# Performance work log

Hardware: AMD Instinct MI355X
Metric: run time of the kernel (lower is better)

The kernel has to match this reference:

```python
import jax, jax.numpy as jnp
import numpy as np

CROP_H = 14
CROP_W = 14
EXTRAPOLATION_VALUE = 0.0


def setup_inputs() -> dict:
    key = jax.random.key(0)
    k1, k2, k3 = jax.random.split(key, 3)
    image = jax.random.normal(k1, (8, 256, 100, 152), dtype=jnp.float32)
    # normalized box coords in [0,1]; (y1,x1,y2,x2), y2<y1 allowed (extrapolation handles it)
    boxes = jax.random.uniform(k2, (1000, 4), dtype=jnp.float32)
    box_ind = jax.random.randint(k3, (1000,), 0, 8, dtype=jnp.int32)
    return {"image": image, "boxes": boxes, "box_ind": box_ind}


def _crop_and_resize(image, boxes, box_ind):
    # image: [B, C, H, W]; boxes: [N, 4] (y1, x1, y2, x2) normalized; box_ind: [N]
    B, C, H, W = image.shape
    dt = image.dtype
    y1, x1, y2, x2 = boxes[:, 0], boxes[:, 1], boxes[:, 2], boxes[:, 3]

    # TF crop_and_resize sampling grid (crop size > 1 path)
    h_scale = (y2 - y1) * (H - 1) / (CROP_H - 1)          # [N]
    w_scale = (x2 - x1) * (W - 1) / (CROP_W - 1)          # [N]
    in_y = y1[:, None] * (H - 1) + jnp.arange(CROP_H, dtype=dt)[None, :] * h_scale[:, None]  # [N, ch]
    in_x = x1[:, None] * (W - 1) + jnp.arange(CROP_W, dtype=dt)[None, :] * w_scale[:, None]  # [N, cw]

    valid_y = (in_y >= 0) & (in_y <= H - 1)               # [N, ch]
    valid_x = (in_x >= 0) & (in_x <= W - 1)               # [N, cw]

    top = jnp.floor(in_y)
    left = jnp.floor(in_x)
    y_lerp = in_y - top                                    # [N, ch]
    x_lerp = in_x - left                                   # [N, cw]

    ti = jnp.clip(top, 0, H - 1).astype(jnp.int32)         # top index    [N, ch]
    bi = jnp.clip(top + 1, 0, H - 1).astype(jnp.int32)     # bottom index [N, ch]
    li = jnp.clip(left, 0, W - 1).astype(jnp.int32)        # left index   [N, cw]
    ri = jnp.clip(left + 1, 0, W - 1).astype(jnp.int32)    # right index  [N, cw]

    b = box_ind[:, None, None]                             # [N, 1, 1]
    yt = ti[:, :, None]
    yb = bi[:, :, None]
    xl = li[:, None, :]
    xr = ri[:, None, :]

    # mixed advanced indexing -> gathered dims first: [N, ch, cw, C]
    tl = image[b, :, yt, xl]
    tr = image[b, :, yt, xr]
    bl = image[b, :, yb, xl]
    br = image[b, :, yb, xr]

    xw = x_lerp[:, None, :, None]                          # [N, 1, cw, 1]
    yw = y_lerp[:, :, None, None]                          # [N, ch, 1, 1]
    top_v = tl + (tr - tl) * xw
    bot_v = bl + (br - bl) * xw
    val = top_v + (bot_v - top_v) * yw                     # [N, ch, cw, C]

    valid = (valid_y[:, :, None] & valid_x[:, None, :])[..., None]
    out = jnp.where(valid, val, jnp.asarray(EXTRAPOLATION_VALUE, dt))
    return jnp.transpose(out, (0, 3, 1, 2))                # [N, C, ch, cw]


def reference(image, boxes, box_ind):
    return _crop_and_resize(image, boxes, box_ind)
```

## Files before the change

### kernel.cpp

```cpp
#include <hip/hip_runtime.h>

#define CROP_H 14
#define CROP_W 14
#define IMG_B 8
#define IMG_C 256
#define IMG_H 100
#define IMG_W 152
#define NBOX 1000
#define PLANE (IMG_H * IMG_W)
#define POS (CROP_H * CROP_W)
#define OUT_PER_BOX (IMG_C * POS)
#define CG 32
#define NCG (IMG_C / CG)

typedef float f2u __attribute__((ext_vector_type(2), aligned(4)));

__global__ __launch_bounds__(1024) void sort_boxes_kernel(
    const int* __restrict__ box_ind,
    int* __restrict__ perm)
{
    __shared__ unsigned s_mask[IMG_B][32];
    __shared__ int s_tot[IMG_B];
    const int tid = threadIdx.x;

    if (tid < IMG_B * 32) ((unsigned*)s_mask)[tid] = 0u;
    __syncthreads();

    int key = 0;
    if (tid < NBOX) {
        key = box_ind[tid];
        atomicOr(&s_mask[key][tid >> 5], 1u << (tid & 31));
    }
    __syncthreads();

    if (tid < IMG_B) {
        int t = 0;
        #pragma unroll
        for (int w = 0; w < 32; ++w) t += __popc(s_mask[tid][w]);
        s_tot[tid] = t;
    }
    __syncthreads();

    if (tid < NBOX) {
        int base = 0;
        #pragma unroll
        for (int k = 0; k < IMG_B; ++k) base += (k < key) ? s_tot[k] : 0;
        const int w = tid >> 5, b = tid & 31;
        int r = __popc(s_mask[key][w] & ((b == 0) ? 0u : ((1u << b) - 1u)));
        for (int ww = 0; ww < w; ++ww) r += __popc(s_mask[key][ww]);
        perm[base + r] = tid;
    }
}

__global__ __launch_bounds__(256) void CropAndResize_16630113370849_kernel(
    const float* __restrict__ image,
    const float* __restrict__ boxes,
    const int* __restrict__ box_ind,
    const int* __restrict__ perm,
    int use_perm,
    float* __restrict__ out)
{
    const int bid  = blockIdx.x;
    const int cg   = bid & 7;
    const int slot = bid >> 3;
    const int tid  = threadIdx.x;
    if (tid >= POS) return;

    const int n = use_perm ? perm[slot] : slot;
    const int b = box_ind[n];

    const int y = tid / CROP_W;
    const int x = tid - y * CROP_W;

    const float y1 = boxes[n * 4 + 0];
    const float x1 = boxes[n * 4 + 1];
    const float y2 = boxes[n * 4 + 2];
    const float x2 = boxes[n * 4 + 3];

    const float hs   = __fdiv_rn(__fmul_rn(__fsub_rn(y2, y1), (float)(IMG_H - 1)),
                                 (float)(CROP_H - 1));
    const float in_y = __fadd_rn(__fmul_rn(y1, (float)(IMG_H - 1)),
                                 __fmul_rn((float)y, hs));
    const int vy = (in_y >= 0.0f) && (in_y <= (float)(IMG_H - 1));
    const float top = floorf(in_y);
    const float yw  = __fsub_rn(in_y, top);
    const int ti = (int)fminf(fmaxf(top, 0.0f), (float)(IMG_H - 1));

    const float ws   = __fdiv_rn(__fmul_rn(__fsub_rn(x2, x1), (float)(IMG_W - 1)),
                                 (float)(CROP_W - 1));
    const float in_x = __fadd_rn(__fmul_rn(x1, (float)(IMG_W - 1)),
                                 __fmul_rn((float)x, ws));
    const int vx = (in_x >= 0.0f) && (in_x <= (float)(IMG_W - 1));
    const float left = floorf(in_x);
    const float xw   = __fsub_rn(in_x, left);
    const int li = (int)fminf(fmaxf(left, 0.0f), (float)(IMG_W - 1));

    const int r0   = min(ti, IMG_H - 2);
    const int c0   = min(li, IMG_W - 2);
    const bool sely = (ti == IMG_H - 1);
    const bool selx = (li == IMG_W - 1);
    const bool vald = (vy & vx) != 0;

    const float* __restrict__ pl =
        image + (size_t)b * (size_t)(IMG_C * PLANE)
              + (size_t)(cg * CG) * PLANE + (r0 * IMG_W + c0);
    float* __restrict__ po =
        out + (size_t)n * (size_t)OUT_PER_BOX + (size_t)(cg * CG) * POS + tid;

    #pragma unroll 8
    for (int cl = 0; cl < CG; ++cl) {
        const f2u ra = *(const f2u*)(pl);
        const f2u rb = *(const f2u*)(pl + IMG_W);

        const float tA = sely ? rb.x : ra.x;
        const float tB = sely ? rb.y : ra.y;
        const float tl = selx ? tB : tA;
        const float bl = selx ? rb.y : rb.x;

        const float top_v = __fadd_rn(tl, __fmul_rn(__fsub_rn(tB, tl), xw));
        const float bot_v = __fadd_rn(bl, __fmul_rn(__fsub_rn(rb.y, bl), xw));
        const float v = __fadd_rn(top_v, __fmul_rn(__fsub_rn(bot_v, top_v), yw));

        __builtin_nontemporal_store(vald ? v : 0.0f, po);
        pl += PLANE;
        po += POS;
    }
}

extern "C" void kernel_launch(void* const* d_in, const int* in_sizes, int n_in,
                              void* d_out, int out_size, void* d_ws, size_t ws_size,
                              hipStream_t stream) {
    const float* image  = (const float*)d_in[0];
    const float* boxes  = (const float*)d_in[1];
    const int*   boxind = (const int*)d_in[2];
    float* out = (float*)d_out;

    const int use_perm = (ws_size >= (size_t)(NBOX * sizeof(int))) ? 1 : 0;
    int* perm = (int*)d_ws;

    if (use_perm) {
        sort_boxes_kernel<<<1, 1024, 0, stream>>>(boxind, perm);
    }

    dim3 grid(NBOX * NCG);
    dim3 block(256);
    CropAndResize_16630113370849_kernel<<<grid, block, 0, stream>>>(
        image, boxes, boxind, perm, use_perm, out);
}
```

Measured before the change: 104.0 us.

## Transpose image to channel-last layout and gather via coalesced HWC crop kernel

Adds a transpose kernel that rewrites the image into a per-64-channel-group HWC layout in workspace. A new crop kernel then gathers the four corner rows as contiguous 64-channel vectors per sample position, with one lane per channel, and stages results in shared memory so the NCHW output stores are coalesced. The aim is to replace the scattered per-channel 8-byte gathers of the old CHW path. The cost is an extra full-image read and write on every call, plus a dependence on a large workspace; if the workspace is too small, the old path runs with plain stores.

```diff
diff --git a/kernel.cpp b/kernel.cpp
--- a/kernel.cpp
+++ b/kernel.cpp
@@ -12,6 +12,9 @@
 #define OUT_PER_BOX (IMG_C * POS)
 #define CG 32
 #define NCG (IMG_C / CG)
+#define G64 4
+#define IMGT_BYTES ((size_t)IMG_B * G64 * PLANE * 64 * 4)
+#define WS_NEED (IMGT_BYTES + NBOX * sizeof(int))
 
 typedef float f2u __attribute__((ext_vector_type(2), aligned(4)));
 
@@ -52,7 +55,140 @@
     }
 }
 
-__global__ __launch_bounds__(256) void CropAndResize_16630113370849_kernel(
+__global__ __launch_bounds__(256) void transpose_kernel(
+    const float* __restrict__ img, float* __restrict__ imgT)
+{
+    __shared__ float tile[64][65];
+    const int pos0 = blockIdx.x * 64;
+    const int g = blockIdx.y, b = blockIdx.z;
+    const int lane = threadIdx.x & 63, warp = threadIdx.x >> 6;
+
+    const int pos_r = pos0 + lane;
+    #pragma unroll
+    for (int i = 0; i < 16; ++i) {
+        const int cl = warp * 16 + i;
+        float v = 0.0f;
+        if (pos_r < PLANE)
+            v = img[((size_t)(b * IMG_C + g * 64 + cl)) * PLANE + pos_r];
+        tile[lane][cl] = v;
+    }
+    __syncthreads();
+    #pragma unroll
+    for (int i = 0; i < 16; ++i) {
+        const int pl = warp * 16 + i;
+        const int pos = pos0 + pl;
+        if (pos < PLANE)
+            imgT[(((size_t)(b * G64 + g)) * PLANE + pos) * 64 + lane] = tile[pl][lane];
+    }
+}
+
+__global__ __launch_bounds__(256) void crop_hwc_kernel(
+    const float* __restrict__ imgT,
+    const float* __restrict__ boxes,
+    const int* __restrict__ box_ind,
+    const int* __restrict__ perm,
+    float* __restrict__ out)
+{
+    __shared__ int   s_pack[POS];
+    __shared__ float s_xw[POS], s_yw[POS];
+    __shared__ float stile[28][65];
+
+    const int bid  = blockIdx.x;
+    const int k    = bid & 7;
+    const int g    = k & 3;
+    const int slot = (k >> 2) * 500 + (bid >> 3);
+    const int tid  = threadIdx.x;
+    const int lane = tid & 63, warp = tid >> 6;
+
+    const int n = perm[slot];
+    const int b = box_ind[n];
+
+    if (tid < POS) {
+        const int y = tid / CROP_W;
+        const int x = tid - y * CROP_W;
+
+        const float y1 = boxes[n * 4 + 0];
+        const float x1 = boxes[n * 4 + 1];
+        const float y2 = boxes[n * 4 + 2];
+        const float x2 = boxes[n * 4 + 3];
+
+        const float hs   = __fdiv_rn(__fmul_rn(__fsub_rn(y2, y1), (float)(IMG_H - 1)),
+                                     (float)(CROP_H - 1));
+        const float in_y = __fadd_rn(__fmul_rn(y1, (float)(IMG_H - 1)),
+                                     __fmul_rn((float)y, hs));
+        const int vy = (in_y >= 0.0f) && (in_y <= (float)(IMG_H - 1));
+        const float top = floorf(in_y);
+        const float ylp = __fsub_rn(in_y, top);
+        const int ti = (int)fminf(fmaxf(top, 0.0f), (float)(IMG_H - 1));
+
+        const float ws   = __fdiv_rn(__fmul_rn(__fsub_rn(x2, x1), (float)(IMG_W - 1)),
+                                     (float)(CROP_W - 1));
+        const float in_x = __fadd_rn(__fmul_rn(x1, (float)(IMG_W - 1)),
+                                     __fmul_rn((float)x, ws));
+        const int vx = (in_x >= 0.0f) && (in_x <= (float)(IMG_W - 1));
+        const float left = floorf(in_x);
+        const float xlp = __fsub_rn(in_x, left);
+        const int li = (int)fminf(fmaxf(left, 0.0f), (float)(IMG_W - 1));
+
+        const int r0   = min(ti, IMG_H - 2);
+        const int c0   = min(li, IMG_W - 2);
+        const int sely = (ti == IMG_H - 1);
+        const int selx = (li == IMG_W - 1);
+        const int off  = r0 * IMG_W + c0;
+
+        s_pack[tid] = off | (selx << 14) | (sely << 15) | (((vy & vx)) << 16);
+        s_xw[tid] = xlp;
+        s_yw[tid] = ylp;
+    }
+    __syncthreads();
+
+    const float* __restrict__ base_img =
+        imgT + ((size_t)(b * G64 + g)) * ((size_t)PLANE * 64);
+    float* __restrict__ out_g =
+        out + (size_t)n * OUT_PER_BOX + (size_t)(g * 64) * POS;
+
+    for (int ch = 0; ch < 7; ++ch) {
+        const int p0 = ch * 28;
+
+        #pragma unroll
+        for (int q = 0; q < 7; ++q) {
+            const int pl = warp * 7 + q;
+            const int p  = p0 + pl;
+            const int w  = s_pack[p];
+            const float xw = s_xw[p], yw = s_yw[p];
+
+            const float* pp  = base_img + (size_t)(w & 0x3FFF) * 64 + lane;
+            const float* pp2 = pp + IMG_W * 64;
+            const float tl0 = pp[0];
+            const float tr0 = pp[64];
+            const float bl  = pp2[0];
+            const float br  = pp2[64];
+
+            const float tA = (w & 0x8000) ? bl : tl0;
+            const float tB = (w & 0x8000) ? br : tr0;
+            const float tl = (w & 0x4000) ? tB : tA;
+            const float blv = (w & 0x4000) ? br : bl;
+
+            const float top_v = __fadd_rn(tl, __fmul_rn(__fsub_rn(tB, tl), xw));
+            const float bot_v = __fadd_rn(blv, __fmul_rn(__fsub_rn(br, blv), xw));
+            const float v = __fadd_rn(top_v, __fmul_rn(__fsub_rn(bot_v, top_v), yw));
+
+            stile[pl][lane] = (w & 0x10000) ? v : 0.0f;
+        }
+        __syncthreads();
+
+        #pragma unroll
+        for (int it = 0; it < 7; ++it) {
+            const int e  = it * 256 + tid;
+            const int cl = e / 28;
+            const int j  = e - cl * 28;
+            out_g[cl * POS + p0 + j] = stile[j][cl];
+        }
+        __syncthreads();
+    }
+}
+
+__global__ __launch_bounds__(256) void crop_chw_kernel(
     const float* __restrict__ image,
     const float* __restrict__ boxes,
     const int* __restrict__ box_ind,
@@ -121,7 +257,7 @@
         const float bot_v = __fadd_rn(bl, __fmul_rn(__fsub_rn(rb.y, bl), xw));
         const float v = __fadd_rn(top_v, __fmul_rn(__fsub_rn(bot_v, top_v), yw));
 
-        __builtin_nontemporal_store(vald ? v : 0.0f, po);
+        *po = vald ? v : 0.0f;
         pl += PLANE;
         po += POS;
     }
@@ -135,15 +271,20 @@
     const int*   boxind = (const int*)d_in[2];
     float* out = (float*)d_out;
 
-    const int use_perm = (ws_size >= (size_t)(NBOX * sizeof(int))) ? 1 : 0;
-    int* perm = (int*)d_ws;
-
-    if (use_perm) {
+    if (ws_size >= WS_NEED) {
+        float* imgT = (float*)d_ws;
+        int*   perm = (int*)((char*)d_ws + IMGT_BYTES);
+
         sort_boxes_kernel<<<1, 1024, 0, stream>>>(boxind, perm);
-    }
-
-    dim3 grid(NBOX * NCG);
-    dim3 block(256);
-    CropAndResize_16630113370849_kernel<<<grid, block, 0, stream>>>(
-        image, boxes, boxind, perm, use_perm, out);
-}
+        transpose_kernel<<<dim3((PLANE + 63) / 64, G64, IMG_B), 256, 0, stream>>>(
+            image, imgT);
+        crop_hwc_kernel<<<dim3(NBOX * G64), 256, 0, stream>>>(
+            imgT, boxes, boxind, perm, out);
+    } else {
+        const int use_perm = (ws_size >= (size_t)(NBOX * sizeof(int))) ? 1 : 0;
+        int* perm = (int*)d_ws;
+        if (use_perm) sort_boxes_kernel<<<1, 1024, 0, stream>>>(boxind, perm);
+        crop_chw_kernel<<<dim3(NBOX * NCG), 256, 0, stream>>>(
+            image, boxes, boxind, perm, use_perm, out);
+    }
+}
```

Result: slower. 197.4 us (+89.8%).

## Stage each image channel plane in LDS and process all boxes per plane

Applied to the files above, without the earlier changes.

The main kernel now runs one block per (channel, image). Each block loads the whole 100x152 channel plane into shared memory, then loops over all boxes belonging to that image, using per-image offsets from the sort kernel, and gathers bilinear taps from LDS. The aim is to read each image plane from global memory once rather than issuing scattered per-box global gathers. The cost is ~60KB of shared memory per block, which limits occupancy, and strided output writes, since each block writes one channel slice per box. Only 2048 blocks are launched, with uneven work across images.

```diff
diff --git a/kernel.cpp b/kernel.cpp
--- a/kernel.cpp
+++ b/kernel.cpp
@@ -10,6 +10,7 @@
 #define PLANE (IMG_H * IMG_W)
 #define POS (CROP_H * CROP_W)
 #define OUT_PER_BOX (IMG_C * POS)
+#define BOXCAP 256
 #define CG 32
 #define NCG (IMG_C / CG)
 
@@ -17,7 +18,8 @@
 
 __global__ __launch_bounds__(1024) void sort_boxes_kernel(
     const int* __restrict__ box_ind,
-    int* __restrict__ perm)
+    int* __restrict__ perm,
+    int* __restrict__ offsets)
 {
     __shared__ unsigned s_mask[IMG_B][32];
     __shared__ int s_tot[IMG_B];
@@ -40,6 +42,13 @@
         s_tot[tid] = t;
     }
     __syncthreads();
+
+    if (tid == 0) {
+        int acc = 0;
+        #pragma unroll
+        for (int k = 0; k < IMG_B; ++k) { offsets[k] = acc; acc += s_tot[k]; }
+        offsets[IMG_B] = acc;
+    }
 
     if (tid < NBOX) {
         int base = 0;
@@ -52,23 +61,115 @@
     }
 }
 
-__global__ __launch_bounds__(256) void CropAndResize_16630113370849_kernel(
+__global__ __launch_bounds__(512, 4) void CropAndResize_16630113370849_kernel(
+    const float* __restrict__ image,
+    const float* __restrict__ boxes,
+    const int* __restrict__ perm,
+    const int* __restrict__ offsets,
+    float* __restrict__ out)
+{
+    __shared__ __align__(16) float s_plane[PLANE];
+    __shared__ float s_hs[BOXCAP], s_ws[BOXCAP], s_y1H[BOXCAP], s_x1W[BOXCAP];
+    __shared__ int   s_n[BOXCAP];
+
+    const int c   = blockIdx.x;
+    const int b   = blockIdx.y;
+    const int tid = threadIdx.x;
+
+    {
+        const float4* __restrict__ src =
+            (const float4*)(image + ((size_t)b * IMG_C + c) * PLANE);
+        float4* dst = (float4*)s_plane;
+        #pragma unroll
+        for (int i = 0; i < 8; ++i) {
+            const int e = i * 512 + tid;
+            if (e < PLANE / 4) dst[e] = src[e];
+        }
+    }
+
+    const int s0 = offsets[b], s1 = offsets[b + 1];
+
+    for (int ck = s0; ck < s1; ck += BOXCAP) {
+        const int cnt = min(BOXCAP, s1 - ck);
+
+        __syncthreads();
+        if (tid < cnt) {
+            const int n = perm[ck + tid];
+            const float y1 = boxes[n * 4 + 0];
+            const float x1 = boxes[n * 4 + 1];
+            const float y2 = boxes[n * 4 + 2];
+            const float x2 = boxes[n * 4 + 3];
+            s_hs[tid]  = __fdiv_rn(__fmul_rn(__fsub_rn(y2, y1), (float)(IMG_H - 1)),
+                                   (float)(CROP_H - 1));
+            s_ws[tid]  = __fdiv_rn(__fmul_rn(__fsub_rn(x2, x1), (float)(IMG_W - 1)),
+                                   (float)(CROP_W - 1));
+            s_y1H[tid] = __fmul_rn(y1, (float)(IMG_H - 1));
+            s_x1W[tid] = __fmul_rn(x1, (float)(IMG_W - 1));
+            s_n[tid]   = n;
+        }
+        __syncthreads();
+
+        const int total = cnt * POS;
+        #pragma unroll 2
+        for (int idx = tid; idx < total; idx += 512) {
+            const int slot = idx / POS;
+            const int p    = idx - slot * POS;
+            const int y    = p / CROP_W;
+            const int x    = p - y * CROP_W;
+
+            const float in_y = __fadd_rn(s_y1H[slot],
+                                         __fmul_rn((float)y, s_hs[slot]));
+            const int vy = (in_y >= 0.0f) && (in_y <= (float)(IMG_H - 1));
+            const float top = floorf(in_y);
+            const float yw  = __fsub_rn(in_y, top);
+            const int ti = (int)fminf(fmaxf(top, 0.0f), (float)(IMG_H - 1));
+
+            const float in_x = __fadd_rn(s_x1W[slot],
+                                         __fmul_rn((float)x, s_ws[slot]));
+            const int vx = (in_x >= 0.0f) && (in_x <= (float)(IMG_W - 1));
+            const float left = floorf(in_x);
+            const float xw   = __fsub_rn(in_x, left);
+            const int li = (int)fminf(fmaxf(left, 0.0f), (float)(IMG_W - 1));
+
+            const int r0 = min(ti, IMG_H - 2);
+            const int c0 = min(li, IMG_W - 2);
+            const bool sely = (ti == IMG_H - 1);
+            const bool selx = (li == IMG_W - 1);
+            const bool vald = (vy & vx) != 0;
+
+            const int off = r0 * IMG_W + c0;
+            const float a0 = s_plane[off];
+            const float a1 = s_plane[off + 1];
+            const float b0 = s_plane[off + IMG_W];
+            const float b1 = s_plane[off + IMG_W + 1];
+
+            const float tA = sely ? b0 : a0;
+            const float tB = sely ? b1 : a1;
+            const float tl = selx ? tB : tA;
+            const float bl = selx ? b1 : b0;
+
+            const float top_v = __fadd_rn(tl, __fmul_rn(__fsub_rn(tB, tl), xw));
+            const float bot_v = __fadd_rn(bl, __fmul_rn(__fsub_rn(b1, bl), xw));
+            const float v = __fadd_rn(top_v, __fmul_rn(__fsub_rn(bot_v, top_v), yw));
+
+            out[(size_t)s_n[slot] * OUT_PER_BOX + c * POS + p] = vald ? v : 0.0f;
+        }
+    }
+}
+
+__global__ __launch_bounds__(256) void crop_chw_kernel(
     const float* __restrict__ image,
     const float* __restrict__ boxes,
     const int* __restrict__ box_ind,
-    const int* __restrict__ perm,
-    int use_perm,
     float* __restrict__ out)
 {
     const int bid  = blockIdx.x;
     const int cg   = bid & 7;
-    const int slot = bid >> 3;
+    const int n    = bid >> 3;
     const int tid  = threadIdx.x;
     if (tid >= POS) return;
 
-    const int n = use_perm ? perm[slot] : slot;
     const int b = box_ind[n];
-
     const int y = tid / CROP_W;
     const int x = tid - y * CROP_W;
 
@@ -95,8 +196,8 @@
     const float xw   = __fsub_rn(in_x, left);
     const int li = (int)fminf(fmaxf(left, 0.0f), (float)(IMG_W - 1));
 
-    const int r0   = min(ti, IMG_H - 2);
-    const int c0   = min(li, IMG_W - 2);
+    const int r0 = min(ti, IMG_H - 2);
+    const int c0 = min(li, IMG_W - 2);
     const bool sely = (ti == IMG_H - 1);
     const bool selx = (li == IMG_W - 1);
     const bool vald = (vy & vx) != 0;
@@ -111,17 +212,14 @@
     for (int cl = 0; cl < CG; ++cl) {
         const f2u ra = *(const f2u*)(pl);
         const f2u rb = *(const f2u*)(pl + IMG_W);
-
         const float tA = sely ? rb.x : ra.x;
         const float tB = sely ? rb.y : ra.y;
         const float tl = selx ? tB : tA;
         const float bl = selx ? rb.y : rb.x;
-
         const float top_v = __fadd_rn(tl, __fmul_rn(__fsub_rn(tB, tl), xw));
         const float bot_v = __fadd_rn(bl, __fmul_rn(__fsub_rn(rb.y, bl), xw));
         const float v = __fadd_rn(top_v, __fmul_rn(__fsub_rn(bot_v, top_v), yw));
-
-        __builtin_nontemporal_store(vald ? v : 0.0f, po);
+        *po = vald ? v : 0.0f;
         pl += PLANE;
         po += POS;
     }
@@ -135,15 +233,16 @@
     const int*   boxind = (const int*)d_in[2];
     float* out = (float*)d_out;
 
-    const int use_perm = (ws_size >= (size_t)(NBOX * sizeof(int))) ? 1 : 0;
-    int* perm = (int*)d_ws;
-
-    if (use_perm) {
-        sort_boxes_kernel<<<1, 1024, 0, stream>>>(boxind, perm);
-    }
-
-    dim3 grid(NBOX * NCG);
-    dim3 block(256);
-    CropAndResize_16630113370849_kernel<<<grid, block, 0, stream>>>(
-        image, boxes, boxind, perm, use_perm, out);
-}
+    const size_t need = (NBOX + IMG_B + 1) * sizeof(int);
+    if (ws_size >= need) {
+        int* perm    = (int*)d_ws;
+        int* offsets = perm + NBOX;
+
+        sort_boxes_kernel<<<1, 1024, 0, stream>>>(boxind, perm, offsets);
+        CropAndResize_16630113370849_kernel<<<dim3(IMG_C, IMG_B), 512, 0, stream>>>(
+            image, boxes, perm, offsets, out);
+    } else {
+        crop_chw_kernel<<<dim3(NBOX * NCG), 256, 0, stream>>>(
+            image, boxes, boxind, out);
+    }
+}
```

Measured after the change: 101.4 us. -2.6%, faster.
